# Optimization experiments

Measured on AMD Instinct MI355X. Metric: run time of the kernel, lower is better.

Reference implementation:

```python
import jax, jax.numpy as jnp
import numpy as np

EPS = 1e-5
D, C, T, H = 512, 256, 2, 2  # d_model, d_ctx, tokens, heads
HD = D // H                   # head dim


def _ln(x, g, b):
    m = x.mean(-1, keepdims=True)
    v = ((x - m) ** 2).mean(-1, keepdims=True)
    return (x - m) / jnp.sqrt(v + EPS) * g + b


def setup_inputs() -> dict:
    key = jax.random.key(0)
    ks = jax.random.split(key, 16)
    B, L = 8, 4096
    w = lambda k, s: (jax.random.normal(k, s, jnp.float32) * 0.02)
    Hc, H2 = 512, 1024  # ctx-head hidden = max(D,C); mix hidden = 2*D
    return {
        "x": jax.random.normal(ks[0], (B, L, D), jnp.float32),
        "context": jax.random.normal(ks[1], (B, C), jnp.float32),
        "pad_valid_mask": jax.random.bernoulli(ks[2], 0.9, (B, L)),
        "film_ln_g": jnp.ones(D), "film_ln_b": jnp.zeros(D),
        "film_w": w(ks[3], (2 * D, C)), "film_b": jnp.zeros(2 * D),
        "concat_w": w(ks[4], (D, D + C)), "concat_b": jnp.zeros(D),
        "concat_ln_g": jnp.ones(D), "concat_ln_b": jnp.zeros(D),
        "ctx_w1": w(ks[5], (Hc, C)), "ctx_b1": jnp.zeros(Hc),
        "ctx_w2": w(ks[6], (T * D, Hc)), "ctx_b2": jnp.zeros(T * D),
        "q_ln_g": jnp.ones(D), "q_ln_b": jnp.zeros(D),
        "in_proj_w": w(ks[7], (3 * D, D)), "in_proj_b": jnp.zeros(3 * D),
        "out_proj_w": w(ks[8], (D, D)), "out_proj_b": jnp.zeros(D),
        "mix_w1": w(ks[9], (H2, 4 * D)), "mix_b1": jnp.zeros(H2),
        "mix_w2": w(ks[10], (D, H2)), "mix_b2": jnp.zeros(D),
        "out_ln_g": jnp.ones(D), "out_ln_b": jnp.zeros(D),
        "gate_w": w(ks[11], (D, C)), "gate_b": jnp.zeros(D),
    }


def reference(x, context, pad_valid_mask,
              film_ln_g, film_ln_b, film_w, film_b,
              concat_w, concat_b, concat_ln_g, concat_ln_b,
              ctx_w1, ctx_b1, ctx_w2, ctx_b2,
              q_ln_g, q_ln_b, in_proj_w, in_proj_b, out_proj_w, out_proj_b,
              mix_w1, mix_b1, mix_w2, mix_b2,
              out_ln_g, out_ln_b, gate_w, gate_b):
    B, L, _ = x.shape
    film_gain, alpha_max = 1.0, 1.0
    # 1) HyperFiLM: base = (1 + gain*gamma) * LN(x) + gain*beta
    gb = context @ film_w.T + film_b                      # [B, 2D]
    gamma, beta = gb[:, :D], gb[:, D:]
    base = (1.0 + film_gain * gamma)[:, None, :] * _ln(x, film_ln_g, film_ln_b) \
           + (film_gain * beta)[:, None, :]
    # 2) Concat path
    ctx_exp = jnp.broadcast_to(context[:, None, :], (B, L, C))
    z = jnp.concatenate([x, ctx_exp], axis=-1)            # [B, L, D+C]
    upd_c = _ln(jax.nn.relu(z @ concat_w.T + concat_b), concat_ln_g, concat_ln_b)
    # 3) Cross-attn path: context -> T tokens
    h = jax.nn.gelu(context @ ctx_w1.T + ctx_b1, approximate=False)
    ctx_tok = (h @ ctx_w2.T + ctx_b2).reshape(B, T, D)
    x_q = _ln(x, q_ln_g, q_ln_b)
    wq, wk, wv = in_proj_w[:D], in_proj_w[D:2 * D], in_proj_w[2 * D:]
    bq, bk, bv = in_proj_b[:D], in_proj_b[D:2 * D], in_proj_b[2 * D:]
    q = (x_q @ wq.T + bq).reshape(B, L, H, HD)
    k = (ctx_tok @ wk.T + bk).reshape(B, T, H, HD)
    v = (ctx_tok @ wv.T + bv).reshape(B, T, H, HD)
    scores = jnp.einsum('blhd,bthd->bhlt', q, k) / jnp.sqrt(jnp.float32(HD))
    attn = jax.nn.softmax(scores, axis=-1)
    a = jnp.einsum('bhlt,bthd->blhd', attn, v).reshape(B, L, D)
    attn_out = a @ out_proj_w.T + out_proj_b
    mix_in = jnp.concatenate([x, attn_out, x - attn_out, x * attn_out], axis=-1)
    upd_a = jax.nn.relu(mix_in @ mix_w1.T + mix_b1) @ mix_w2.T + mix_b2
    # 4) Combine with sigmoid gate, alpha, pad mask
    gate = jax.nn.sigmoid(context @ gate_w.T + gate_b) * alpha_max  # [B, D]
    gate = gate[:, None, :] * pad_valid_mask[:, :, None].astype(x.dtype)
    out = _ln(base + gate * (upd_c + upd_a), out_ln_g, out_ln_b)
    return out
```

## Files before the change

### kernel.cpp

```cpp
#include <hip/hip_runtime.h>
#include <hip/hip_bf16.h>


#define N_TOK 32768
#define HALF_ROWS 16384

typedef unsigned short u16;
typedef __attribute__((ext_vector_type(8))) __bf16 bf16x8;
typedef __attribute__((ext_vector_type(4))) float f32x4;

__device__ __forceinline__ float bf2f(unsigned int h) { return __uint_as_float(h << 16); }
__device__ __forceinline__ u16 f2bf(float f) {
    unsigned int u = __float_as_uint(f);
    u += 0x7FFFu + ((u >> 16) & 1u);
    return (u16)(u >> 16);
}
__device__ __forceinline__ void load8(const u16* p, float* v) {
    uint4 u = *(const uint4*)p;
    v[0] = bf2f(u.x & 0xffffu); v[1] = bf2f(u.x >> 16);
    v[2] = bf2f(u.y & 0xffffu); v[3] = bf2f(u.y >> 16);
    v[4] = bf2f(u.z & 0xffffu); v[5] = bf2f(u.z >> 16);
    v[6] = bf2f(u.w & 0xffffu); v[7] = bf2f(u.w >> 16);
}
__device__ __forceinline__ uint4 pack8(const float* v) {
    uint4 u;
    u.x = (unsigned)f2bf(v[0]) | ((unsigned)f2bf(v[1]) << 16);
    u.y = (unsigned)f2bf(v[2]) | ((unsigned)f2bf(v[3]) << 16);
    u.z = (unsigned)f2bf(v[4]) | ((unsigned)f2bf(v[5]) << 16);
    u.w = (unsigned)f2bf(v[6]) | ((unsigned)f2bf(v[7]) << 16);
    return u;
}
__device__ __forceinline__ void async16(const u16* g, u16* lds) {
    __builtin_amdgcn_global_load_lds(
        (const __attribute__((address_space(1))) unsigned int*)g,
        (__attribute__((address_space(3))) unsigned int*)lds, 16, 0, 0);
}

#define FENCE() asm volatile("" ::: "memory")
#define BARRIER() do { FENCE(); __builtin_amdgcn_s_barrier(); FENCE(); } while (0)
#define WAITV(n) asm volatile("s_waitcnt vmcnt(" #n ")" ::: "memory")
#define LGKM0()  asm volatile("s_waitcnt lgkmcnt(0)" ::: "memory")


__device__ void prep_body(unsigned bid, int tid,
                          const float* __restrict__ in_proj_w,
                          const float* __restrict__ in_proj_b,
                          const float* __restrict__ qb,
                          const float* __restrict__ concat_w,
                          const float* __restrict__ mix_w1,
                          const float* __restrict__ mix_w2,
                          const float* __restrict__ context,
                          float* __restrict__ bqp,
                          u16* __restrict__ cwbf, u16* __restrict__ m1bf,
                          u16* __restrict__ m2bf, u16* __restrict__ ctxbf) {
    if (bid < 128) {
        const int wave = tid >> 6, lane = tid & 63;
        const int j = bid * 4 + wave;
        const int i = lane * 8;
        float4 w0 = *(const float4*)(in_proj_w + (size_t)j * 512 + i);
        float4 w1 = *(const float4*)(in_proj_w + (size_t)j * 512 + i + 4);
        float4 b0 = *(const float4*)(qb + i);
        float4 b1 = *(const float4*)(qb + i + 4);
        float p1 = w0.x*b0.x + w0.y*b0.y + w0.z*b0.z + w0.w*b0.w
                 + w1.x*b1.x + w1.y*b1.y + w1.z*b1.z + w1.w*b1.w;
        for (int m = 1; m < 64; m <<= 1) p1 += __shfl_xor(p1, m, 64);
        if (lane == 0) bqp[j] = in_proj_b[j] + p1;
    } else if (bid < 320) {
        int i = (bid - 128) * 256 + tid;
        const float* s = concat_w + (size_t)i * 8;
        float4 a = *(const float4*)s;
        float4 b = *(const float4*)(s + 4);
        float v[8] = {a.x, a.y, a.z, a.w, b.x, b.y, b.z, b.w};
        *(uint4*)(cwbf + (size_t)i * 8) = pack8(v);
    } else if (bid < 576) {
        int i = (bid - 320) * 256 + tid;
        const float* s = mix_w2 + (size_t)i * 8;
        float4 a = *(const float4*)s;
        float4 b = *(const float4*)(s + 4);
        float v[8] = {a.x, a.y, a.z, a.w, b.x, b.y, b.z, b.w};
        *(uint4*)(m2bf + (size_t)i * 8) = pack8(v);
    } else if (bid < 1344) {
        int idx = (bid - 576) * 256 + tid;
        int n = idx / 192;
        int k = (idx - n * 192) * 8;
        const float* base = mix_w1 + (size_t)n * 2048;
        float v[8];
        if (k < 512) {
            #pragma unroll
            for (int e = 0; e < 8; e++) v[e] = base[k + e] + base[1024 + k + e];
        } else if (k < 1024) {
            #pragma unroll
            for (int e = 0; e < 8; e++) v[e] = base[k + e] - base[512 + k + e];
        } else {
            #pragma unroll
            for (int e = 0; e < 8; e++) v[e] = base[512 + k + e];
        }
        *(uint4*)(m1bf + (size_t)n * 1536 + k) = pack8(v);
    } else {
        for (int i = tid; i < 2048; i += 256)
            ctxbf[i] = f2bf(context[i]);
    }
}

__device__ void ctx_a_body(unsigned task, int tid,
                           const float* __restrict__ context,
                           const float* __restrict__ film_w, const float* __restrict__ film_b,
                           const float* __restrict__ gate_w, const float* __restrict__ gate_b,
                           const float* __restrict__ ctx_w1, const float* __restrict__ ctx_b1,
                           float* __restrict__ gb1, float* __restrict__ betab,
                           float* __restrict__ gateb, float* __restrict__ hbuf) {
    const int wave = tid >> 6, lane = tid & 63;
    const int widx = (int)task * 4 + wave;
    const int b   = widx >> 11;
    const int j2  = widx & 2047;
    const int cat = j2 >> 9;
    const int j   = j2 & 511;
    const float* wrow;
    if      (cat == 0) wrow = film_w + (size_t)j * 256;
    else if (cat == 1) wrow = film_w + (size_t)(512 + j) * 256;
    else if (cat == 2) wrow = gate_w + (size_t)j * 256;
    else               wrow = ctx_w1 + (size_t)j * 256;
    float4 wv = *(const float4*)(wrow + lane * 4);
    float4 cv = *(const float4*)(context + b * 256 + lane * 4);
    float s = wv.x * cv.x + wv.y * cv.y + wv.z * cv.z + wv.w * cv.w;
    for (int m = 1; m < 64; m <<= 1) s += __shfl_xor(s, m, 64);
    if (lane == 0) {
        if      (cat == 0) gb1[b * 512 + j]   = 1.0f + s + film_b[j];
        else if (cat == 1) betab[b * 512 + j] = s + film_b[512 + j];
        else if (cat == 2) gateb[b * 512 + j] = 1.f / (1.f + expf(-(s + gate_b[j])));
        else {
            float hv = s + ctx_b1[j];
            hbuf[b * 512 + j] = 0.5f * hv * (1.0f + erff(hv * 0.70710678118654752f));
        }
    }
}

__global__ void prep_ctxa_kernel(const float* __restrict__ in_proj_w,
                                 const float* __restrict__ in_proj_b,
                                 const float* __restrict__ qb,
                                 const float* __restrict__ concat_w,
                                 const float* __restrict__ mix_w1,
                                 const float* __restrict__ mix_w2,
                                 const float* __restrict__ context,
                                 float* __restrict__ bqp,
                                 u16* __restrict__ cwbf, u16* __restrict__ m1bf,
                                 u16* __restrict__ m2bf, u16* __restrict__ ctxbf,
                                 const float* __restrict__ film_w, const float* __restrict__ film_b,
                                 const float* __restrict__ gate_w, const float* __restrict__ gate_b,
                                 const float* __restrict__ ctx_w1, const float* __restrict__ ctx_b1,
                                 float* __restrict__ gb1, float* __restrict__ betab,
                                 float* __restrict__ gateb, float* __restrict__ hbuf) {
    if (blockIdx.x < 1345)
        prep_body(blockIdx.x, threadIdx.x, in_proj_w, in_proj_b, qb, concat_w,
                  mix_w1, mix_w2, context, bqp, cwbf, m1bf, m2bf, ctxbf);
    else
        ctx_a_body(blockIdx.x - 1345, threadIdx.x, context, film_w, film_b,
                   gate_w, gate_b, ctx_w1, ctx_b1, gb1, betab, gateb, hbuf);
}

__global__ void ctx_stage_b(const float* __restrict__ hbuf,
                            const float* __restrict__ ctx_w2, const float* __restrict__ ctx_b2,
                            float* __restrict__ tokbuf) {
    const int wave = threadIdx.x >> 6, lane = threadIdx.x & 63;
    const int widx = blockIdx.x * 4 + wave;
    const int b = widx >> 10;
    const int j = widx & 1023;
    const float* wrow = ctx_w2 + (size_t)j * 512 + lane * 8;
    const float* hr   = hbuf + b * 512 + lane * 8;
    float4 w0 = *(const float4*)wrow, w1 = *(const float4*)(wrow + 4);
    float4 h0 = *(const float4*)hr,   h1 = *(const float4*)(hr + 4);
    float s = w0.x*h0.x + w0.y*h0.y + w0.z*h0.z + w0.w*h0.w
            + w1.x*h1.x + w1.y*h1.y + w1.z*h1.z + w1.w*h1.w;
    for (int m = 1; m < 64; m <<= 1) s += __shfl_xor(s, m, 64);
    if (lane == 0) tokbuf[b * 1024 + j] = s + ctx_b2[j];
}

__global__ void ctx_stage_c(const float* __restrict__ tokbuf,
                            const float* __restrict__ in_proj_w, const float* __restrict__ in_proj_b,
                            float* __restrict__ kbuf, float* __restrict__ vbuf) {
    const int wave = threadIdx.x >> 6, lane = threadIdx.x & 63;
    const int widx = blockIdx.x * 4 + wave;
    const int b  = widx >> 11;
    const int r  = widx & 2047;
    const int t  = r >> 10;
    const int kv = (r >> 9) & 1;
    const int j  = r & 511;
    const float* wrow = in_proj_w + (size_t)(512 + kv * 512 + j) * 512 + lane * 8;
    const float* tk   = tokbuf + (b * 2 + t) * 512 + lane * 8;
    float4 w0 = *(const float4*)wrow, w1 = *(const float4*)(wrow + 4);
    float4 t0 = *(const float4*)tk,   t1 = *(const float4*)(tk + 4);
    float s = w0.x*t0.x + w0.y*t0.y + w0.z*t0.z + w0.w*t0.w
            + w1.x*t1.x + w1.y*t1.y + w1.z*t1.z + w1.w*t1.w;
    for (int m = 1; m < 64; m <<= 1) s += __shfl_xor(s, m, 64);
    if (lane == 0) {
        float v = s + in_proj_b[512 + kv * 512 + j];
        if (kv == 0) kbuf[(b * 2 + t) * 512 + j] = v;
        else         vbuf[(b * 2 + t) * 512 + j] = v;
    }
}

__global__ void ctx_stage_d(const float* __restrict__ in_proj_w,
                            const float* __restrict__ out_proj_w,
                            const float* __restrict__ qg, const float* __restrict__ bqp,
                            const float* __restrict__ kbuf, const float* __restrict__ vbuf,
                            float* __restrict__ ubuf, float* __restrict__ vobuf,
                            float* __restrict__ subuf, float* __restrict__ c0buf) {
    const int tid = threadIdx.x;
    __shared__ float sh[256];
    __shared__ float red[256];
    if (blockIdx.x < 32) {
        const int bid = blockIdx.x;
        const int b = bid >> 2, idx = bid & 3;
        const int t = idx >> 1, h = idx & 1;
        sh[tid] = kbuf[(b * 2 + t) * 512 + h * 256 + tid];
        __syncthreads();
        float a0 = 0.f, a1 = 0.f;
        #pragma unroll 4
        for (int dd = 0; dd < 256; dd++) {
            const float kv = sh[dd];
            const float* wr = in_proj_w + (size_t)(h * 256 + dd) * 512;
            a0 += kv * wr[tid];
            a1 += kv * wr[tid + 256];
        }
        float u0 = a0 * qg[tid], u1 = a1 * qg[tid + 256];
        ubuf[bid * 512 + tid]       = u0;
        ubuf[bid * 512 + tid + 256] = u1;
        red[tid] = u0 + u1;
        __syncthreads();
        for (int s = 128; s > 0; s >>= 1) { if (tid < s) red[tid] += red[tid + s]; __syncthreads(); }
        if (tid == 0) subuf[bid] = red[0];
        __syncthreads();
        red[tid] = bqp[h * 256 + tid] * sh[tid];
        __syncthreads();
        for (int s = 128; s > 0; s >>= 1) { if (tid < s) red[tid] += red[tid + s]; __syncthreads(); }
        if (tid == 0) c0buf[bid] = red[0];
    } else {
        const int bid = blockIdx.x - 32;
        const int b = bid >> 2, idx = bid & 3;
        const int t = idx >> 1, h = idx & 1;
        sh[tid] = vbuf[(b * 2 + t) * 512 + h * 256 + tid];
        __syncthreads();
        const float* w0 = out_proj_w + (size_t)tid * 512 + h * 256;
        const float* w1 = out_proj_w + (size_t)(tid + 256) * 512 + h * 256;
        float acc0 = 0.f, acc1 = 0.f;
        #pragma unroll 2
        for (int dd = 0; dd < 256; dd += 4) {
            float4 x0 = *(const float4*)(w0 + dd);
            float4 x1 = *(const float4*)(w1 + dd);
            acc0 += x0.x*sh[dd] + x0.y*sh[dd+1] + x0.z*sh[dd+2] + x0.w*sh[dd+3];
            acc1 += x1.x*sh[dd] + x1.y*sh[dd+1] + x1.z*sh[dd+2] + x1.w*sh[dd+3];
        }
        vobuf[bid * 512 + tid]       = acc0;
        vobuf[bid * 512 + tid + 256] = acc1;
    }
}

__global__ void statsattn_kernel(const float* __restrict__ x, float* __restrict__ stats,
                                 u16* __restrict__ mixA, u16* __restrict__ pbufH,
                                 const float* __restrict__ ubuf, const float* __restrict__ subuf,
                                 const float* __restrict__ c0buf, const float* __restrict__ vobuf,
                                 const float* __restrict__ ob, const int rowbase) {
    const int wave = threadIdx.x >> 6, lane = threadIdx.x & 63;
    const size_t lr = (size_t)blockIdx.x * 8 + wave * 2;
    const size_t gr = lr + rowbase;
    const int b = (int)(gr >> 12);
    float v[2][8], s[2] = {0.f, 0.f}, ss[2] = {0.f, 0.f};
    #pragma unroll
    for (int r = 0; r < 2; r++) {
        const float* xr = x + (gr + r) * 512 + lane * 8;
        float4 a = *(const float4*)xr;
        float4 c = *(const float4*)(xr + 4);
        v[r][0]=a.x; v[r][1]=a.y; v[r][2]=a.z; v[r][3]=a.w;
        v[r][4]=c.x; v[r][5]=c.y; v[r][6]=c.z; v[r][7]=c.w;
        #pragma unroll
        for (int e = 0; e < 8; e++) { s[r] += v[r][e]; ss[r] += v[r][e] * v[r][e]; }
    }
    float u[4][8];
    #pragma unroll
    for (int idx = 0; idx < 4; idx++) {
        const float* up = ubuf + (b * 4 + idx) * 512 + lane * 8;
        float4 u0 = *(const float4*)up, u1 = *(const float4*)(up + 4);
        u[idx][0]=u0.x; u[idx][1]=u0.y; u[idx][2]=u0.z; u[idx][3]=u0.w;
        u[idx][4]=u1.x; u[idx][5]=u1.y; u[idx][6]=u1.z; u[idx][7]=u1.w;
    }
    float sd[2][4];
    #pragma unroll
    for (int r = 0; r < 2; r++)
        #pragma unroll
        for (int idx = 0; idx < 4; idx++) {
            float acc = 0.f;
            #pragma unroll
            for (int e = 0; e < 8; e++) acc += v[r][e] * u[idx][e];
            sd[r][idx] = acc;
        }
    for (int m = 1; m < 64; m <<= 1) {
        #pragma unroll
        for (int r = 0; r < 2; r++) {
            s[r] += __shfl_xor(s[r], m, 64); ss[r] += __shfl_xor(ss[r], m, 64);
            #pragma unroll
            for (int idx = 0; idx < 4; idx++) sd[r][idx] += __shfl_xor(sd[r][idx], m, 64);
        }
    }
    float vo[4][8];
    #pragma unroll
    for (int idx = 0; idx < 4; idx++) {
        const float* vp = vobuf + (b * 4 + idx) * 512 + lane * 8;
        float4 v0 = *(const float4*)vp, v1 = *(const float4*)(vp + 4);
        vo[idx][0]=v0.x; vo[idx][1]=v0.y; vo[idx][2]=v0.z; vo[idx][3]=v0.w;
        vo[idx][4]=v1.x; vo[idx][5]=v1.y; vo[idx][6]=v1.z; vo[idx][7]=v1.w;
    }
    float obp[8];
    {
        const float* op = ob + lane * 8;
        float4 o0 = *(const float4*)op, o1 = *(const float4*)(op + 4);
        obp[0]=o0.x; obp[1]=o0.y; obp[2]=o0.z; obp[3]=o0.w;
        obp[4]=o1.x; obp[5]=o1.y; obp[6]=o1.z; obp[7]=o1.w;
    }
    #pragma unroll
    for (int r = 0; r < 2; r++) {
        const float mean = s[r] * (1.f / 512.f);
        const float rstd = rsqrtf(ss[r] * (1.f / 512.f) - mean * mean + 1e-5f);
        if (lane == 0) { stats[(gr + r) * 2] = mean; stats[(gr + r) * 2 + 1] = rstd; }
        float sc[4];
        #pragma unroll
        for (int idx = 0; idx < 4; idx++)
            sc[idx] = (rstd * (sd[r][idx] - mean * subuf[b * 4 + idx]) + c0buf[b * 4 + idx]) * (1.f / 16.f);
        float p[4];
        #pragma unroll
        for (int h = 0; h < 2; h++) {
            float s0 = sc[h], s1 = sc[2 + h];
            float mx = fmaxf(s0, s1);
            float e0 = expf(s0 - mx), e1 = expf(s1 - mx);
            float inv = 1.f / (e0 + e1);
            p[h] = e0 * inv; p[2 + h] = e1 * inv;
        }
        float o[8], pr[8];
        #pragma unroll
        for (int e = 0; e < 8; e++) {
            o[e] = p[0]*vo[0][e] + p[1]*vo[1][e] + p[2]*vo[2][e] + p[3]*vo[3][e] + obp[e];
            pr[e] = v[r][e] * o[e];
        }
        *(uint4*)(mixA + (gr + r) * 1024 + lane * 8)       = pack8(v[r]);
        *(uint4*)(mixA + (gr + r) * 1024 + 512 + lane * 8) = pack8(o);
        *(uint4*)(pbufH + (lr + r) * 512 + lane * 8)       = pack8(pr);
    }
}

template<int AMODE, int NT, bool RELU>
__launch_bounds__(512, 2)
__global__ void mix_gemm8(const u16* __restrict__ A0, const u16* __restrict__ A1,
                          const u16* __restrict__ Wb, const float* __restrict__ bias,
                          u16* __restrict__ out, const int ldo) {
    constexpr int BLD = NT * 64;
    constexpr int NIT = NT / 2;
    extern __shared__ __align__(16) u16 S[];
    u16* As = S;
    u16* Bs = S + 32768;
    const int tid = threadIdx.x;
    const int l = tid & 63;
    const int w = tid >> 6;
    const int wm = w >> 2, wn = w & 3;
    const int quad = l >> 4, lc = l & 15;
    const size_t m0 = (size_t)blockIdx.x * 256;
    const int n0 = blockIdx.y * 256;
    const int bidx = (int)(m0 >> 12);

    const int r0 = tid >> 3;
    const int r1 = (tid + 512) >> 3;
    const int c0s = ((tid & 7) ^ (r0 & 7)) * 8;
    const int c1s = ((tid & 7) ^ (r1 & 7)) * 8;

    auto stA = [&](int kt, int h, int buf) {
        u16* dst = As + (buf * 2 + h) * 8192;
        if constexpr (AMODE == 0) {
            async16(A0 + (m0 + h * 128 + r0) * 1024 + kt * 64 + c0s, dst + tid * 8);
            async16(A0 + (m0 + h * 128 + r1) * 1024 + kt * 64 + c1s, dst + (tid + 512) * 8);
        } else if constexpr (AMODE == 1) {
            if (kt < 8) {
                async16(A0 + (m0 + h * 128 + r0) * 1024 + kt * 64 + c0s, dst + tid * 8);
                async16(A0 + (m0 + h * 128 + r1) * 1024 + kt * 64 + c1s, dst + (tid + 512) * 8);
            } else {
                async16(A1 + bidx * 256 + (kt - 8) * 64 + c0s, dst + tid * 8);
                async16(A1 + bidx * 256 + (kt - 8) * 64 + c1s, dst + (tid + 512) * 8);
            }
        } else {
            if (kt < 16) {
                async16(A0 + (m0 + h * 128 + r0) * 1024 + kt * 64 + c0s, dst + tid * 8);
                async16(A0 + (m0 + h * 128 + r1) * 1024 + kt * 64 + c1s, dst + (tid + 512) * 8);
            } else {
                async16(A1 + (m0 + h * 128 + r0) * 512 + (kt - 16) * 64 + c0s, dst + tid * 8);
                async16(A1 + (m0 + h * 128 + r1) * 512 + (kt - 16) * 64 + c1s, dst + (tid + 512) * 8);
            }
        }
    };
    auto stB = [&](int kt, int h, int buf) {
        u16* dst = Bs + (buf * 2 + h) * 8192;
        async16(Wb + (size_t)(n0 + h * 128 + r0) * BLD + kt * 64 + c0s, dst + tid * 8);
        async16(Wb + (size_t)(n0 + h * 128 + r1) * BLD + kt * 64 + c1s, dst + (tid + 512) * 8);
    };

    bf16x8 a_[4][2], b_[2][2][2];
    f32x4 acc[8][4];
    #pragma unroll
    for (int i = 0; i < 8; i++)
        #pragma unroll
        for (int j = 0; j < 4; j++) acc[i][j] = (f32x4){0.f, 0.f, 0.f, 0.f};

    auto rdA = [&](int buf, int qi) {
        const u16* Ab = As + (buf * 2 + wm) * 8192;
        #pragma unroll
        for (int ii = 0; ii < 4; ii++) {
            const int r = (qi * 4 + ii) * 16 + lc;
            #pragma unroll
            for (int kk = 0; kk < 2; kk++) {
                const int cs = (kk * 4 + quad) ^ (r & 7);
                a_[ii][kk] = *(const bf16x8*)&Ab[r * 64 + cs * 8];
            }
        }
    };
    auto rdB = [&](int buf, int qj) {
        #pragma unroll
        for (int jj = 0; jj < 2; jj++) {
            const int nr = wn * 64 + (qj * 2 + jj) * 16 + lc;
            const int hb = nr >> 7, r = nr & 127;
            const u16* Bb = Bs + (buf * 2 + hb) * 8192;
            #pragma unroll
            for (int kk = 0; kk < 2; kk++) {
                const int cs = (kk * 4 + quad) ^ (r & 7);
                b_[qj][jj][kk] = *(const bf16x8*)&Bb[r * 64 + cs * 8];
            }
        }
    };
    auto mfma16 = [&](int qi, int qj) {
        __builtin_amdgcn_s_setprio(1);
        #pragma unroll
        for (int ii = 0; ii < 4; ii++)
            #pragma unroll
            for (int jj = 0; jj < 2; jj++)
                #pragma unroll
                for (int kk = 0; kk < 2; kk++)
                    acc[qi * 4 + ii][qj * 2 + jj] = __builtin_amdgcn_mfma_f32_16x16x32_bf16(
                        a_[ii][kk], b_[qj][jj][kk], acc[qi * 4 + ii][qj * 2 + jj], 0, 0, 0);
        __builtin_amdgcn_s_setprio(0);
    };

    stA(0, 0, 0); stA(0, 1, 0); stB(0, 0, 0); stB(0, 1, 0);
    stB(1, 0, 1); stB(1, 1, 1);
    WAITV(4); BARRIER();

    for (int it = 0; it < NIT; it++) {
        const int t0 = 2 * it, t1 = 2 * it + 1;
        const bool more = (it + 1 < NIT);
        rdA(0, 0); rdB(0, 0);
        stA(t1, 0, 1);
        BARRIER(); mfma16(0, 0);
        rdB(0, 1);
        stA(t1, 1, 1);
        BARRIER(); mfma16(0, 1);
        BARRIER();
        rdA(0, 1);
        if (more) stB(t0 + 2, 0, 0);
        BARRIER(); mfma16(1, 1);
        if (more) { stB(t0 + 2, 1, 0); WAITV(4); }
        else      { WAITV(0); }
        BARRIER(); mfma16(1, 0);
        rdA(1, 0); rdB(1, 0);
        if (more) stA(t0 + 2, 0, 0);
        BARRIER(); mfma16(0, 0);
        rdB(1, 1);
        if (more) stA(t0 + 2, 1, 0);
        BARRIER(); mfma16(0, 1);
        BARRIER();
        rdA(1, 1);
        if (more) stB(t1 + 2, 0, 1);
        BARRIER(); mfma16(1, 1);
        if (more) { stB(t1 + 2, 1, 1); WAITV(4); }
        BARRIER(); mfma16(1, 0);
    }

    BARRIER();
    float bv[4];
    #pragma unroll
    for (int j = 0; j < 4; j++) bv[j] = bias[n0 + wn * 64 + j * 16 + lc];
    #pragma unroll
    for (int p = 0; p < 2; p++) {
        if (p) BARRIER();
        if (wm == p) {
            #pragma unroll
            for (int i = 0; i < 8; i++)
                #pragma unroll
                for (int j = 0; j < 4; j++)
                    #pragma unroll
                    for (int reg = 0; reg < 4; reg++) {
                        float vv = acc[i][j][reg] + bv[j];
                        if (RELU) vv = fmaxf(vv, 0.f);
                        S[(i * 16 + quad * 4 + reg) * 264 + wn * 64 + j * 16 + lc] = f2bf(vv);
                    }
        }
        LGKM0(); BARRIER();
        #pragma unroll
        for (int kq = 0; kq < 8; kq++) {
            const int cix = tid + kq * 512;
            const int row = cix >> 5, ch = cix & 31;
            *(uint4*)(out + (m0 + p * 128 + row) * (size_t)ldo + n0 + ch * 8)
                = *(const uint4*)&S[row * 264 + ch * 8];
        }
    }
}

__global__ void final_kernel(const u16* __restrict__ mixA, const float* __restrict__ stats,
                             const u16* __restrict__ bufc,
                             const float* __restrict__ cg_, const float* __restrict__ cb,
                             const float* __restrict__ gb1, const float* __restrict__ betab,
                             const float* __restrict__ gateb, const int* __restrict__ mask,
                             const float* __restrict__ fg, const float* __restrict__ fb,
                             const float* __restrict__ og, const float* __restrict__ ob,
                             float* __restrict__ out) {
    const int wave = threadIdx.x >> 6, lane = threadIdx.x & 63;
    const size_t row = (size_t)blockIdx.x * 4 + wave;
    const int b = (int)(row >> 12);
    const int c0 = lane * 8;
    float xv[8], uc[8], ua[8];
    load8(mixA + row * 1024 + c0, xv);
    load8(mixA + row * 1024 + 512 + c0, ua);
    load8(bufc + row * 512 + c0, uc);
    float sc = 0.f, ssc = 0.f;
    #pragma unroll
    for (int e = 0; e < 8; e++) { sc += uc[e]; ssc += uc[e] * uc[e]; }
    for (int m = 1; m < 64; m <<= 1) { sc += __shfl_xor(sc, m, 64); ssc += __shfl_xor(ssc, m, 64); }
    const float mc = sc * (1.f / 512.f);
    const float rc = rsqrtf(ssc * (1.f / 512.f) - mc * mc + 1e-5f);
    const float mean = stats[row * 2], rstd = stats[row * 2 + 1];
    const float mf = (mask[row] != 0) ? 1.f : 0.f;
    float y[8];
    float s = 0.f, ss = 0.f;
    #pragma unroll
    for (int e = 0; e < 8; e++) {
        int c = c0 + e;
        float ucn = (uc[e] - mc) * rc * cg_[c] + cb[c];
        float xh = (xv[e] - mean) * rstd;
        float base = gb1[b * 512 + c] * (xh * fg[c] + fb[c]) + betab[b * 512 + c];
        float yv = base + gateb[b * 512 + c] * mf * (ucn + ua[e]);
        y[e] = yv; s += yv; ss += yv * yv;
    }
    for (int m = 1; m < 64; m <<= 1) { s += __shfl_xor(s, m, 64); ss += __shfl_xor(ss, m, 64); }
    float mean2 = s * (1.f / 512.f);
    float rstd2 = rsqrtf(ss * (1.f / 512.f) - mean2 * mean2 + 1e-5f);
    float o[8];
    #pragma unroll
    for (int e = 0; e < 8; e++) {
        int c = c0 + e;
        o[e] = (y[e] - mean2) * rstd2 * og[c] + ob[c];
    }
    *(float4*)(out + row * 512 + c0)     = make_float4(o[0], o[1], o[2], o[3]);
    *(float4*)(out + row * 512 + c0 + 4) = make_float4(o[4], o[5], o[6], o[7]);
}

extern "C" void kernel_launch(void* const* d_in, const int* in_sizes, int n_in,
                              void* d_out, int out_size, void* d_ws, size_t ws_size,
                              hipStream_t stream) {
    const float* x          = (const float*)d_in[0];
    const float* context    = (const float*)d_in[1];
    const int*   mask       = (const int*)d_in[2];
    const float* film_ln_g  = (const float*)d_in[3];
    const float* film_ln_b  = (const float*)d_in[4];
    const float* film_w     = (const float*)d_in[5];
    const float* film_b     = (const float*)d_in[6];
    const float* concat_w   = (const float*)d_in[7];
    const float* concat_b   = (const float*)d_in[8];
    const float* concat_ln_g= (const float*)d_in[9];
    const float* concat_ln_b= (const float*)d_in[10];
    const float* ctx_w1     = (const float*)d_in[11];
    const float* ctx_b1     = (const float*)d_in[12];
    const float* ctx_w2     = (const float*)d_in[13];
    const float* ctx_b2     = (const float*)d_in[14];
    const float* q_ln_g     = (const float*)d_in[15];
    const float* q_ln_b     = (const float*)d_in[16];
    const float* in_proj_w  = (const float*)d_in[17];
    const float* in_proj_b  = (const float*)d_in[18];
    const float* out_proj_w = (const float*)d_in[19];
    const float* out_proj_b = (const float*)d_in[20];
    const float* mix_w1     = (const float*)d_in[21];
    const float* mix_b1     = (const float*)d_in[22];
    const float* mix_w2     = (const float*)d_in[23];
    const float* mix_b2     = (const float*)d_in[24];
    const float* out_ln_g   = (const float*)d_in[25];
    const float* out_ln_b   = (const float*)d_in[26];
    const float* gate_w     = (const float*)d_in[27];
    const float* gate_b     = (const float*)d_in[28];
    float* out = (float*)d_out;

    float* gb1    = (float*)d_ws;
    float* betab  = gb1 + 4096;
    float* gateb  = betab + 4096;
    float* kbuf   = gateb + 4096;
    float* vbuf   = kbuf + 8192;
    float* bqp    = vbuf + 8192;
    float* hbuf   = bqp + 512;
    float* tokbuf = hbuf + 4096;
    float* ubuf   = tokbuf + 8192;
    float* vobuf  = ubuf + 16384;
    float* subuf  = vobuf + 16384;
    float* c0buf  = subuf + 32;
    float* stats  = c0buf + 32;
    u16* ctxbf = (u16*)(stats + 65536);
    u16* cwbf  = ctxbf + 2048;
    u16* m1bf  = cwbf + 393216;
    u16* m2bf  = m1bf + 1572864;
    u16* mixA  = m2bf + 524288;
    u16* bufh  = mixA + (size_t)N_TOK * 1024;
    u16* bufc  = bufh;
    u16* pbufH = bufh + (size_t)N_TOK * 1024;

    static bool attr_set = false;
    if (!attr_set) {
        hipFuncSetAttribute(reinterpret_cast<const void*>(&mix_gemm8<2, 24, true>),
                            hipFuncAttributeMaxDynamicSharedMemorySize, 131072);
        hipFuncSetAttribute(reinterpret_cast<const void*>(&mix_gemm8<0, 16, false>),
                            hipFuncAttributeMaxDynamicSharedMemorySize, 131072);
        hipFuncSetAttribute(reinterpret_cast<const void*>(&mix_gemm8<1, 12, true>),
                            hipFuncAttributeMaxDynamicSharedMemorySize, 131072);
        attr_set = true;
    }

    prep_ctxa_kernel<<<5441, 256, 0, stream>>>(
        in_proj_w, in_proj_b, q_ln_b, concat_w, mix_w1, mix_w2, context,
        bqp, cwbf, m1bf, m2bf, ctxbf,
        film_w, film_b, gate_w, gate_b, ctx_w1, ctx_b1,
        gb1, betab, gateb, hbuf);
    ctx_stage_b<<<2048, 256, 0, stream>>>(hbuf, ctx_w2, ctx_b2, tokbuf);
    ctx_stage_c<<<4096, 256, 0, stream>>>(tokbuf, in_proj_w, in_proj_b, kbuf, vbuf);
    ctx_stage_d<<<64, 256, 0, stream>>>(in_proj_w, out_proj_w, q_ln_g, bqp,
                                        kbuf, vbuf, ubuf, vobuf, subuf, c0buf);

    for (int h = 0; h < 2; h++) {
        const int rowbase = h * HALF_ROWS;
        statsattn_kernel<<<HALF_ROWS / 8, 256, 0, stream>>>(
            x, stats, mixA, pbufH, ubuf, subuf, c0buf, vobuf, out_proj_b, rowbase);
        mix_gemm8<2, 24, true><<<dim3(64, 4), 512, 131072, stream>>>(
            mixA + (size_t)rowbase * 1024, pbufH, m1bf, mix_b1,
            bufh + (size_t)rowbase * 1024, 1024);
    }
    mix_gemm8<0, 16, false><<<dim3(128, 2), 512, 131072, stream>>>(
        bufh, nullptr, m2bf, mix_b2, mixA + 512, 1024);

    mix_gemm8<1, 12, true><<<dim3(128, 2), 512, 131072, stream>>>(
        mixA, ctxbf, cwbf, concat_b, bufc, 512);

    final_kernel<<<N_TOK / 4, 256, 0, stream>>>(mixA, stats, bufc,
                                                concat_ln_g, concat_ln_b,
                                                gb1, betab, gateb, mask,
                                                film_ln_g, film_ln_b,
                                                out_ln_g, out_ln_b, out);
    (void)in_sizes; (void)n_in; (void)out_size; (void)ws_size;
}
```

Before: 424.9 us.

## Merge mix2 and concat GEMMs, drop half-split when workspace allows, reorder GEMM prefetch

Splits ctx_stage_d across twice as many blocks, with atomic accumulation into subuf, which is now zeroed in the prep kernel. When the workspace is large enough, it runs statsattn and the first mix GEMM over all tokens at once instead of two halves, and fuses the mix2 and concat GEMMs into one launch with a 256x2 grid. The GEMM body's prefetch schedule is reordered to stage A and B tiles differently, waiting on vmcnt(2) instead of vmcnt(4). This cuts launch count and tail effects and fills more CUs, at the cost of a larger workspace and a more complex pipeline schedule.

Result: faster. 414.9 us (-2.3%).

```diff
diff --git a/kernel.cpp b/kernel.cpp
--- a/kernel.cpp
+++ b/kernel.cpp
@@ -40,7 +40,6 @@
 #define BARRIER() do { FENCE(); __builtin_amdgcn_s_barrier(); FENCE(); } while (0)
 #define WAITV(n) asm volatile("s_waitcnt vmcnt(" #n ")" ::: "memory")
 #define LGKM0()  asm volatile("s_waitcnt lgkmcnt(0)" ::: "memory")
-
 
 __device__ void prep_body(unsigned bid, int tid,
                           const float* __restrict__ in_proj_w,
@@ -52,7 +51,8 @@
                           const float* __restrict__ context,
                           float* __restrict__ bqp,
                           u16* __restrict__ cwbf, u16* __restrict__ m1bf,
-                          u16* __restrict__ m2bf, u16* __restrict__ ctxbf) {
+                          u16* __restrict__ m2bf, u16* __restrict__ ctxbf,
+                          float* __restrict__ subuf) {
     if (bid < 128) {
         const int wave = tid >> 6, lane = tid & 63;
         const int j = bid * 4 + wave;
@@ -99,6 +99,7 @@
     } else {
         for (int i = tid; i < 2048; i += 256)
             ctxbf[i] = f2bf(context[i]);
+        if (tid < 32) subuf[tid] = 0.f;
     }
 }
 
@@ -145,6 +146,7 @@
                                  float* __restrict__ bqp,
                                  u16* __restrict__ cwbf, u16* __restrict__ m1bf,
                                  u16* __restrict__ m2bf, u16* __restrict__ ctxbf,
+                                 float* __restrict__ subuf,
                                  const float* __restrict__ film_w, const float* __restrict__ film_b,
                                  const float* __restrict__ gate_w, const float* __restrict__ gate_b,
                                  const float* __restrict__ ctx_w1, const float* __restrict__ ctx_b1,
@@ -152,7 +154,7 @@
                                  float* __restrict__ gateb, float* __restrict__ hbuf) {
     if (blockIdx.x < 1345)
         prep_body(blockIdx.x, threadIdx.x, in_proj_w, in_proj_b, qb, concat_w,
-                  mix_w1, mix_w2, context, bqp, cwbf, m1bf, m2bf, ctxbf);
+                  mix_w1, mix_w2, context, bqp, cwbf, m1bf, m2bf, ctxbf, subuf);
     else
         ctx_a_body(blockIdx.x - 1345, threadIdx.x, context, film_w, film_b,
                    gate_w, gate_b, ctx_w1, ctx_b1, gb1, betab, gateb, hbuf);
@@ -199,59 +201,55 @@
     }
 }
 
-__global__ void ctx_stage_d(const float* __restrict__ in_proj_w,
-                            const float* __restrict__ out_proj_w,
-                            const float* __restrict__ qg, const float* __restrict__ bqp,
-                            const float* __restrict__ kbuf, const float* __restrict__ vbuf,
-                            float* __restrict__ ubuf, float* __restrict__ vobuf,
-                            float* __restrict__ subuf, float* __restrict__ c0buf) {
+__global__ void ctx_stage_d2(const float* __restrict__ in_proj_w,
+                             const float* __restrict__ out_proj_w,
+                             const float* __restrict__ qg, const float* __restrict__ bqp,
+                             const float* __restrict__ kbuf, const float* __restrict__ vbuf,
+                             float* __restrict__ ubuf, float* __restrict__ vobuf,
+                             float* __restrict__ subuf, float* __restrict__ c0buf) {
     const int tid = threadIdx.x;
     __shared__ float sh[256];
     __shared__ float red[256];
-    if (blockIdx.x < 32) {
-        const int bid = blockIdx.x;
-        const int b = bid >> 2, idx = bid & 3;
+    if (blockIdx.x < 64) {
+        const int task = blockIdx.x >> 1, jh = blockIdx.x & 1;
+        const int b = task >> 2, idx = task & 3;
         const int t = idx >> 1, h = idx & 1;
+        const int j = jh * 256 + tid;
         sh[tid] = kbuf[(b * 2 + t) * 512 + h * 256 + tid];
         __syncthreads();
-        float a0 = 0.f, a1 = 0.f;
+        float a = 0.f;
         #pragma unroll 4
-        for (int dd = 0; dd < 256; dd++) {
-            const float kv = sh[dd];
-            const float* wr = in_proj_w + (size_t)(h * 256 + dd) * 512;
-            a0 += kv * wr[tid];
-            a1 += kv * wr[tid + 256];
-        }
-        float u0 = a0 * qg[tid], u1 = a1 * qg[tid + 256];
-        ubuf[bid * 512 + tid]       = u0;
-        ubuf[bid * 512 + tid + 256] = u1;
-        red[tid] = u0 + u1;
+        for (int dd = 0; dd < 256; dd++)
+            a += sh[dd] * in_proj_w[(size_t)(h * 256 + dd) * 512 + j];
+        float u = a * qg[j];
+        ubuf[task * 512 + j] = u;
+        red[tid] = u;
         __syncthreads();
         for (int s = 128; s > 0; s >>= 1) { if (tid < s) red[tid] += red[tid + s]; __syncthreads(); }
-        if (tid == 0) subuf[bid] = red[0];
-        __syncthreads();
-        red[tid] = bqp[h * 256 + tid] * sh[tid];
-        __syncthreads();
-        for (int s = 128; s > 0; s >>= 1) { if (tid < s) red[tid] += red[tid + s]; __syncthreads(); }
-        if (tid == 0) c0buf[bid] = red[0];
+        if (tid == 0) atomicAdd(&subuf[task], red[0]);
+        if (jh == 0) {
+            __syncthreads();
+            red[tid] = bqp[h * 256 + tid] * sh[tid];
+            __syncthreads();
+            for (int s = 128; s > 0; s >>= 1) { if (tid < s) red[tid] += red[tid + s]; __syncthreads(); }
+            if (tid == 0) c0buf[task] = red[0];
+        }
     } else {
-        const int bid = blockIdx.x - 32;
-        const int b = bid >> 2, idx = bid & 3;
+        const int r = blockIdx.x - 64;
+        const int task = r >> 1, jh = r & 1;
+        const int b = task >> 2, idx = task & 3;
         const int t = idx >> 1, h = idx & 1;
+        const int j = jh * 256 + tid;
         sh[tid] = vbuf[(b * 2 + t) * 512 + h * 256 + tid];
         __syncthreads();
-        const float* w0 = out_proj_w + (size_t)tid * 512 + h * 256;
-        const float* w1 = out_proj_w + (size_t)(tid + 256) * 512 + h * 256;
-        float acc0 = 0.f, acc1 = 0.f;
+        const float* w0 = out_proj_w + (size_t)j * 512 + h * 256;
+        float acc0 = 0.f;
         #pragma unroll 2
         for (int dd = 0; dd < 256; dd += 4) {
             float4 x0 = *(const float4*)(w0 + dd);
-            float4 x1 = *(const float4*)(w1 + dd);
             acc0 += x0.x*sh[dd] + x0.y*sh[dd+1] + x0.z*sh[dd+2] + x0.w*sh[dd+3];
-            acc1 += x1.x*sh[dd] + x1.y*sh[dd+1] + x1.z*sh[dd+2] + x1.w*sh[dd+3];
-        }
-        vobuf[bid * 512 + tid]       = acc0;
-        vobuf[bid * 512 + tid + 256] = acc1;
+        }
+        vobuf[task * 512 + j] = acc0;
     }
 }
 
@@ -347,13 +345,12 @@
 }
 
 template<int AMODE, int NT, bool RELU>
-__launch_bounds__(512, 2)
-__global__ void mix_gemm8(const u16* __restrict__ A0, const u16* __restrict__ A1,
-                          const u16* __restrict__ Wb, const float* __restrict__ bias,
-                          u16* __restrict__ out, const int ldo) {
+__device__ __forceinline__ void gemm8_body(const u16* __restrict__ A0, const u16* __restrict__ A1,
+                                           const u16* __restrict__ Wb, const float* __restrict__ bias,
+                                           u16* __restrict__ out, const int ldo,
+                                           const int bx, const int by, u16* S) {
     constexpr int BLD = NT * 64;
     constexpr int NIT = NT / 2;
-    extern __shared__ __align__(16) u16 S[];
     u16* As = S;
     u16* Bs = S + 32768;
     const int tid = threadIdx.x;
@@ -361,8 +358,8 @@
     const int w = tid >> 6;
     const int wm = w >> 2, wn = w & 3;
     const int quad = l >> 4, lc = l & 15;
-    const size_t m0 = (size_t)blockIdx.x * 256;
-    const int n0 = blockIdx.y * 256;
+    const size_t m0 = (size_t)bx * 256;
+    const int n0 = by * 256;
     const int bidx = (int)(m0 >> 12);
 
     const int r0 = tid >> 3;
@@ -445,36 +442,36 @@
     };
 
     stA(0, 0, 0); stA(0, 1, 0); stB(0, 0, 0); stB(0, 1, 0);
-    stB(1, 0, 1); stB(1, 1, 1);
-    WAITV(4); BARRIER();
+    stA(1, 0, 1);
+    WAITV(2); BARRIER();
 
     for (int it = 0; it < NIT; it++) {
-        const int t0 = 2 * it, t1 = 2 * it + 1;
-        const bool more = (it + 1 < NIT);
+        const int tb = 2 * it + 1;
+        const bool more = (it < NIT - 1);
         rdA(0, 0); rdB(0, 0);
-        stA(t1, 0, 1);
+        stA(tb, 1, 1);
         BARRIER(); mfma16(0, 0);
         rdB(0, 1);
-        stA(t1, 1, 1);
+        stB(tb, 0, 1);
         BARRIER(); mfma16(0, 1);
+        rdA(0, 1);
+        stB(tb, 1, 1);
+        BARRIER(); mfma16(1, 1);
         BARRIER();
-        rdA(0, 1);
-        if (more) stB(t0 + 2, 0, 0);
-        BARRIER(); mfma16(1, 1);
-        if (more) { stB(t0 + 2, 1, 0); WAITV(4); }
+        if (more) { stA(tb + 1, 0, 0); WAITV(2); }
         else      { WAITV(0); }
         BARRIER(); mfma16(1, 0);
         rdA(1, 0); rdB(1, 0);
-        if (more) stA(t0 + 2, 0, 0);
+        if (more) stA(tb + 1, 1, 0);
         BARRIER(); mfma16(0, 0);
         rdB(1, 1);
-        if (more) stA(t0 + 2, 1, 0);
+        if (more) stB(tb + 1, 0, 0);
         BARRIER(); mfma16(0, 1);
+        rdA(1, 1);
+        if (more) stB(tb + 1, 1, 0);
+        BARRIER(); mfma16(1, 1);
         BARRIER();
-        rdA(1, 1);
-        if (more) stB(t1 + 2, 0, 1);
-        BARRIER(); mfma16(1, 1);
-        if (more) { stB(t1 + 2, 1, 1); WAITV(4); }
+        if (more) { stA(tb + 2, 0, 1); WAITV(2); }
         BARRIER(); mfma16(1, 0);
     }
 
@@ -506,6 +503,30 @@
                 = *(const uint4*)&S[row * 264 + ch * 8];
         }
     }
+}
+
+template<int AMODE, int NT, bool RELU>
+__launch_bounds__(512, 2)
+__global__ void mix_gemm8(const u16* __restrict__ A0, const u16* __restrict__ A1,
+                          const u16* __restrict__ Wb, const float* __restrict__ bias,
+                          u16* __restrict__ out, const int ldo) {
+    extern __shared__ __align__(16) u16 S[];
+    gemm8_body<AMODE, NT, RELU>(A0, A1, Wb, bias, out, ldo, blockIdx.x, blockIdx.y, S);
+}
+
+__launch_bounds__(512, 2)
+__global__ void mix2_concat_kernel(const u16* __restrict__ bufh, const u16* __restrict__ m2bf,
+                                   const float* __restrict__ mix_b2, u16* __restrict__ out_a,
+                                   const u16* __restrict__ mixA, const u16* __restrict__ ctxbf,
+                                   const u16* __restrict__ cwbf, const float* __restrict__ concat_b,
+                                   u16* __restrict__ bufc) {
+    extern __shared__ __align__(16) u16 S[];
+    if (blockIdx.x < 128)
+        gemm8_body<0, 16, false>(bufh, nullptr, m2bf, mix_b2, out_a, 1024,
+                                 blockIdx.x, blockIdx.y, S);
+    else
+        gemm8_body<1, 12, true>(mixA, ctxbf, cwbf, concat_b, bufc, 512,
+                                blockIdx.x - 128, blockIdx.y, S);
 }
 
 __global__ void final_kernel(const u16* __restrict__ mixA, const float* __restrict__ stats,
@@ -609,8 +630,9 @@
     u16* m2bf  = m1bf + 1572864;
     u16* mixA  = m2bf + 524288;
     u16* bufh  = mixA + (size_t)N_TOK * 1024;
-    u16* bufc  = bufh;
-    u16* pbufH = bufh + (size_t)N_TOK * 1024;
+    u16* pbuf  = bufh + (size_t)N_TOK * 1024;
+
+    const bool full = (ws_size >= 173316352ull);
 
     static bool attr_set = false;
     if (!attr_set) {
@@ -620,37 +642,54 @@
                             hipFuncAttributeMaxDynamicSharedMemorySize, 131072);
         hipFuncSetAttribute(reinterpret_cast<const void*>(&mix_gemm8<1, 12, true>),
                             hipFuncAttributeMaxDynamicSharedMemorySize, 131072);
+        hipFuncSetAttribute(reinterpret_cast<const void*>(&mix2_concat_kernel),
+                            hipFuncAttributeMaxDynamicSharedMemorySize, 131072);
         attr_set = true;
     }
 
     prep_ctxa_kernel<<<5441, 256, 0, stream>>>(
         in_proj_w, in_proj_b, q_ln_b, concat_w, mix_w1, mix_w2, context,
-        bqp, cwbf, m1bf, m2bf, ctxbf,
+        bqp, cwbf, m1bf, m2bf, ctxbf, subuf,
         film_w, film_b, gate_w, gate_b, ctx_w1, ctx_b1,
         gb1, betab, gateb, hbuf);
     ctx_stage_b<<<2048, 256, 0, stream>>>(hbuf, ctx_w2, ctx_b2, tokbuf);
     ctx_stage_c<<<4096, 256, 0, stream>>>(tokbuf, in_proj_w, in_proj_b, kbuf, vbuf);
-    ctx_stage_d<<<64, 256, 0, stream>>>(in_proj_w, out_proj_w, q_ln_g, bqp,
-                                        kbuf, vbuf, ubuf, vobuf, subuf, c0buf);
-
-    for (int h = 0; h < 2; h++) {
-        const int rowbase = h * HALF_ROWS;
-        statsattn_kernel<<<HALF_ROWS / 8, 256, 0, stream>>>(
-            x, stats, mixA, pbufH, ubuf, subuf, c0buf, vobuf, out_proj_b, rowbase);
-        mix_gemm8<2, 24, true><<<dim3(64, 4), 512, 131072, stream>>>(
-            mixA + (size_t)rowbase * 1024, pbufH, m1bf, mix_b1,
-            bufh + (size_t)rowbase * 1024, 1024);
-    }
-    mix_gemm8<0, 16, false><<<dim3(128, 2), 512, 131072, stream>>>(
-        bufh, nullptr, m2bf, mix_b2, mixA + 512, 1024);
-
-    mix_gemm8<1, 12, true><<<dim3(128, 2), 512, 131072, stream>>>(
-        mixA, ctxbf, cwbf, concat_b, bufc, 512);
-
-    final_kernel<<<N_TOK / 4, 256, 0, stream>>>(mixA, stats, bufc,
-                                                concat_ln_g, concat_ln_b,
-                                                gb1, betab, gateb, mask,
-                                                film_ln_g, film_ln_b,
-                                                out_ln_g, out_ln_b, out);
+    ctx_stage_d2<<<128, 256, 0, stream>>>(in_proj_w, out_proj_w, q_ln_g, bqp,
+                                          kbuf, vbuf, ubuf, vobuf, subuf, c0buf);
+
+    if (full) {
+        u16* bufc = pbuf;
+        statsattn_kernel<<<N_TOK / 8, 256, 0, stream>>>(
+            x, stats, mixA, pbuf, ubuf, subuf, c0buf, vobuf, out_proj_b, 0);
+        mix_gemm8<2, 24, true><<<dim3(128, 4), 512, 131072, stream>>>(
+            mixA, pbuf, m1bf, mix_b1, bufh, 1024);
+        mix2_concat_kernel<<<dim3(256, 2), 512, 131072, stream>>>(
+            bufh, m2bf, mix_b2, mixA + 512,
+            mixA, ctxbf, cwbf, concat_b, bufc);
+        final_kernel<<<N_TOK / 4, 256, 0, stream>>>(mixA, stats, bufc,
+                                                    concat_ln_g, concat_ln_b,
+                                                    gb1, betab, gateb, mask,
+                                                    film_ln_g, film_ln_b,
+                                                    out_ln_g, out_ln_b, out);
+    } else {
+        u16* bufc = bufh;
+        for (int h = 0; h < 2; h++) {
+            const int rowbase = h * HALF_ROWS;
+            statsattn_kernel<<<HALF_ROWS / 8, 256, 0, stream>>>(
+                x, stats, mixA, pbuf, ubuf, subuf, c0buf, vobuf, out_proj_b, rowbase);
+            mix_gemm8<2, 24, true><<<dim3(64, 4), 512, 131072, stream>>>(
+                mixA + (size_t)rowbase * 1024, pbuf, m1bf, mix_b1,
+                bufh + (size_t)rowbase * 1024, 1024);
+        }
+        mix_gemm8<0, 16, false><<<dim3(128, 2), 512, 131072, stream>>>(
+            bufh, nullptr, m2bf, mix_b2, mixA + 512, 1024);
+        mix_gemm8<1, 12, true><<<dim3(128, 2), 512, 131072, stream>>>(
+            mixA, ctxbf, cwbf, concat_b, bufc, 512);
+        final_kernel<<<N_TOK / 4, 256, 0, stream>>>(mixA, stats, bufc,
+                                                    concat_ln_g, concat_ln_b,
+                                                    gb1, betab, gateb, mask,
+                                                    film_ln_g, film_ln_b,
+                                                    out_ln_g, out_ln_b, out);
+    }
     (void)in_sizes; (void)n_in; (void)out_size; (void)ws_size;
 }
```
